# Kernel optimization log

Measured on AMD Instinct MI355X. Metric: run time of the kernel, lower is better.

## Reference

```python
import jax, jax.numpy as jnp
import numpy as np

EPS = 1e-12


def _pchip_slopes(y, x):
    """PCHIP (Fritsch-Carlson) slopes. y: (S, K), x: (K) -> (S, K)."""
    K = y.shape[-1]
    if K < 2:
        return jnp.zeros_like(y)
    h = x[1:] - x[:-1]                              # (K-1,)
    delta = (y[..., 1:] - y[..., :-1]) / (h + EPS)  # (S, K-1)
    if K == 2:
        return jnp.broadcast_to(delta[..., :1], y.shape).astype(y.dtype)
    # interior slopes: weighted harmonic mean where secants agree in sign
    delta_prev = delta[..., :-1]
    delta_next = delta[..., 1:]
    same_sign = delta_prev * delta_next > 0
    h_prev = h[:-1]
    h_next = h[1:]
    w1 = 2.0 * h_next + h_prev
    w2 = h_next + 2.0 * h_prev
    denom = w1 / (delta_prev + EPS) + w2 / (delta_next + EPS)
    d_int = (w1 + w2) / (denom + EPS)
    d_mid = jnp.where(same_sign, d_int, jnp.zeros_like(d_int))  # (S, K-2)
    # left endpoint (one-sided, shape-limited)
    h0, h1 = h[0], h[1]
    delta0 = delta[..., 0]
    delta1 = delta[..., 1]
    d0 = ((2.0 * h0 + h1) * delta0 - h0 * delta1) / (h0 + h1 + EPS)
    d0 = jnp.where(jnp.sign(d0) != jnp.sign(delta0), jnp.zeros_like(d0), d0)
    d0 = jnp.where((jnp.sign(delta0) != jnp.sign(delta1)) & (jnp.abs(d0) > 3.0 * jnp.abs(delta0)), 3.0 * delta0, d0)
    # right endpoint
    hn1, hn2 = h[-1], h[-2]
    deltan1 = delta[..., -1]
    deltan2 = delta[..., -2]
    dn = ((2.0 * hn1 + hn2) * deltan1 - hn1 * deltan2) / (hn1 + hn2 + EPS)
    dn = jnp.where(jnp.sign(dn) != jnp.sign(deltan1), jnp.zeros_like(dn), dn)
    dn = jnp.where((jnp.sign(deltan1) != jnp.sign(deltan2)) & (jnp.abs(dn) > 3.0 * jnp.abs(deltan1)), 3.0 * deltan1, dn)
    return jnp.concatenate([d0[..., None], d_mid, dn[..., None]], axis=-1)


def setup_inputs() -> dict:
    key = jax.random.key(0)
    k1, k2 = jax.random.split(key)
    B, S, K = 4096, 4096, 64
    x_min, x_max = -3.0, 3.0
    xq = jax.random.normal(k1, (B, S), dtype=jnp.float32) * 2.0  # some queries outside domain
    coeffs = jax.random.normal(k2, (S, K), dtype=jnp.float32)
    knots = jnp.linspace(x_min, x_max, K, dtype=jnp.float32)
    return {"xq": xq, "coeffs": coeffs, "knots": knots}


def reference(xq, coeffs, knots):
    y = coeffs                                   # (S, K)
    d = _pchip_slopes(y, knots)                  # (S, K)
    K = knots.shape[0]
    x0_dom = knots[0]
    x1_dom = knots[-1]
    below = xq < x0_dom
    above = xq > x1_dom
    xq_c = jnp.clip(xq, x0_dom, x1_dom)
    idx = jnp.searchsorted(knots, xq_c) - 1      # (B, S) interval index
    idx = jnp.clip(idx, 0, K - 2)
    x0 = knots[idx]
    x1 = knots[idx + 1]
    h = x1 - x0 + EPS
    t = (xq_c - x0) / h
    t2 = t * t
    t3 = t2 * t
    h00 = 2.0 * t3 - 3.0 * t2 + 1.0
    h10 = t3 - 2.0 * t2 + t
    h01 = -2.0 * t3 + 3.0 * t2
    h11 = t3 - t2
    s_idx = jnp.arange(y.shape[0])[None, :]      # (1, S) spline index
    y0 = y[s_idx, idx]
    y1 = y[s_idx, idx + 1]
    d0 = d[s_idx, idx]
    d1 = d[s_idx, idx + 1]
    interp = h00 * y0 + h10 * h * d0 + h01 * y1 + h11 * h * d1
    out = jnp.where(below, y[None, :, 0] + d[None, :, 0] * (xq - x0_dom), interp)
    out = jnp.where(above, y[None, :, -1] + d[None, :, -1] * (xq - x1_dom), out)
    return out
```

## Files before the change

### kernel.cpp

```cpp
#include <hip/hip_runtime.h>

#define EPSF 1e-12f
#define STILE 64
#define KK 64
#define RSTR 65
#define FSTR (4 * RSTR)
#define BLK 1024
#define NWAVE (BLK / 64)
#define PRELOOP ((STILE * KK) / BLK)

__device__ __forceinline__ float sgnf(float x) {
    return (x > 0.f) ? 1.f : ((x < 0.f) ? -1.f : 0.f);
}

__device__ __forceinline__ float4 eval4(float4 xv, const float4* __restrict__ qb,
                                        float af, float bf) {
    float xs[4] = {xv.x, xv.y, xv.z, xv.w};
    float t[4], ext[4];
    float4 c[4];
#pragma unroll
    for (int j = 0; j < 4; j++) {
        float tf = fmaf(xs[j], af, bf);
        float tc = fminf(fmaxf(tf, 0.f), (float)(KK - 1));
        int id = min((int)tc, KK - 2);
        t[j] = tc - (float)id;
        ext[j] = tf - tc;
        c[j] = qb[j * RSTR + id];
    }
    float r[4];
#pragma unroll
    for (int j = 0; j < 4; j++) {
        float P = fmaf(fmaf(fmaf(c[j].w, t[j], c[j].z), t[j], c[j].y), t[j], c[j].x);
        float w = fmaf(fmaf(t[j], 2.f, t[j]), c[j].w, c[j].z + c[j].z);
        float Pp = fmaf(t[j], w, c[j].y);
        r[j] = fmaf(Pp, ext[j], P);
    }
    return make_float4(r[0], r[1], r[2], r[3]);
}

__global__ __launch_bounds__(BLK, 8) void pchip_fused4(
    const float* __restrict__ xq,
    const float* __restrict__ coeffs,
    const float* __restrict__ knots,
    float* __restrict__ out,
    int S, int b_chunk)
{
    __shared__ float4 cf4[STILE * RSTR];
    __shared__ float skn[KK];
    float* cf = (float*)cf4;

    int tid = threadIdx.x;
    int s0 = blockIdx.x * STILE;
    int b0 = blockIdx.y * b_chunk;

    if (tid < KK) skn[tid] = knots[tid];
#pragma unroll
    for (int i = 0; i < PRELOOP; i++) {
        int p = tid + i * BLK;
        int sl = p >> 6, k = p & 63;
        cf[sl * FSTR + 4 * k] = coeffs[(size_t)(s0 + sl) * KK + k];
    }
    __syncthreads();
#pragma unroll
    for (int i = 0; i < PRELOOP; i++) {
        int p = tid + i * BLK;
        int sl = p >> 6, k = p & 63;
        if (k < KK - 1) {
            int ib = sl * FSTR + 4 * k;
            float hh = skn[k + 1] - skn[k];
            cf[ib + 3] = (cf[ib + 4] - cf[ib]) / (hh + EPSF);
        }
    }
    __syncthreads();
#pragma unroll
    for (int i = 0; i < PRELOOP; i++) {
        int p = tid + i * BLK;
        int sl = p >> 6, k = p & 63;
        int rb = sl * FSTR;
        float d;
        if (k == 0) {
            float h0 = skn[1] - skn[0], h1 = skn[2] - skn[1];
            float de0 = cf[rb + 3], de1 = cf[rb + 7];
            d = ((2.f * h0 + h1) * de0 - h0 * de1) / (h0 + h1 + EPSF);
            if (sgnf(d) != sgnf(de0)) d = 0.f;
            if ((sgnf(de0) != sgnf(de1)) && (fabsf(d) > 3.f * fabsf(de0))) d = 3.f * de0;
        } else if (k == KK - 1) {
            float hn1 = skn[KK - 1] - skn[KK - 2], hn2 = skn[KK - 2] - skn[KK - 3];
            float dn1 = cf[rb + 4 * (KK - 2) + 3], dn2 = cf[rb + 4 * (KK - 3) + 3];
            d = ((2.f * hn1 + hn2) * dn1 - hn1 * dn2) / (hn1 + hn2 + EPSF);
            if (sgnf(d) != sgnf(dn1)) d = 0.f;
            if ((sgnf(dn1) != sgnf(dn2)) && (fabsf(d) > 3.f * fabsf(dn1))) d = 3.f * dn1;
        } else {
            float dprev = cf[rb + 4 * (k - 1) + 3], dnext = cf[rb + 4 * k + 3];
            float hp = skn[k] - skn[k - 1], hn = skn[k + 1] - skn[k];
            bool same = dprev * dnext > 0.f;
            float w1 = 2.f * hn + hp;
            float w2 = hn + 2.f * hp;
            float denom = w1 / (dprev + EPSF) + w2 / (dnext + EPSF);
            float dint = (w1 + w2) / (denom + EPSF);
            d = same ? dint : 0.f;
        }
        cf[rb + 4 * k + 2] = d;
    }
    __syncthreads();
    float c1r[PRELOOP], c2r[PRELOOP], c3r[PRELOOP];
#pragma unroll
    for (int i = 0; i < PRELOOP; i++) {
        int p = tid + i * BLK;
        int sl = p >> 6, k = p & 63;
        int kc = min(k, KK - 2);
        int ib = sl * FSTR + 4 * kc;
        float y0 = cf[ib], y1 = cf[ib + 4];
        float d0 = cf[ib + 2], d1 = cf[ib + 6];
        float h = skn[kc + 1] - skn[kc] + EPSF;
        c1r[i] = h * d0;
        c2r[i] = 3.f * (y1 - y0) - h * (2.f * d0 + d1);
        c3r[i] = 2.f * (y0 - y1) + h * (d0 + d1);
    }
    __syncthreads();
#pragma unroll
    for (int i = 0; i < PRELOOP; i++) {
        int p = tid + i * BLK;
        int sl = p >> 6, k = p & 63;
        if (k < KK - 1) {
            int ib = sl * FSTR + 4 * k;
            cf[ib + 1] = c1r[i];
            cf[ib + 2] = c2r[i];
            cf[ib + 3] = c3r[i];
        }
    }
    __syncthreads();

    float x0d = skn[0], x1d = skn[KK - 1];
    float invh = (float)(KK - 1) / (x1d - x0d);
    float af = invh, bf = -x0d * invh;
    int wv = tid >> 6, lane = tid & 63;
    int cgrp = (lane & 15) << 2;
    int brw = lane >> 4;
    const float4* qb = cf4 + cgrp * RSTR;

    int rpw = b_chunk / NWAVE;
    int nb = rpw >> 2;
    size_t off = (size_t)(b0 + wv * rpw + brw) * S + s0 + cgrp;
    const size_t step = (size_t)4 * S;

    float4 xa = *(const float4*)(xq + off);
    float4 xb = *(const float4*)(xq + (nb > 1 ? off + step : off));
    for (int ii = 0; ii < nb; ii++) {
        float4 xn = *(const float4*)(xq + (ii + 2 < nb ? off + 2 * step : off));
        float4 r = eval4(xa, qb, af, bf);
        *(float4*)(out + off) = r;
        xa = xb; xb = xn;
        off += step;
    }
}

extern "C" void kernel_launch(void* const* d_in, const int* in_sizes, int n_in,
                              void* d_out, int out_size, void* d_ws, size_t ws_size,
                              hipStream_t stream) {
    const float* xq     = (const float*)d_in[0];
    const float* coeffs = (const float*)d_in[1];
    const float* knots  = (const float*)d_in[2];
    float* out = (float*)d_out;

    int K = in_sizes[2];
    int S = in_sizes[1] / K;
    int N = in_sizes[0];
    int B = N / S;

    int n_btiles = 8;
    int b_chunk = B / n_btiles;
    dim3 grid(S / STILE, n_btiles);
    pchip_fused4<<<grid, BLK, 0, stream>>>(xq, coeffs, knots, out, S, b_chunk);
}
```

Baseline: 126.9 us.

## Widen spline tile and software-pipeline LDS coefficient gathers with nontemporal stores

Doubles the spline tile to 128 columns so each wave covers 128 contiguous floats per row in two rows instead of four. The main loop is restructured so the interval index and LDS coefficient gather for the next row are issued before the Horner evaluation of the current one, with a scheduling barrier between them. Outputs are written with nontemporal stores. This is meant to hide LDS and global latency and reduce cache pollution, but it doubles LDS per block, so each CU holds fewer blocks, and it raises register pressure.

New measurement: 130.0 us. 2.4% more time.

```diff
diff --git a/kernel.cpp b/kernel.cpp
--- a/kernel.cpp
+++ b/kernel.cpp
@@ -1,7 +1,7 @@
 #include <hip/hip_runtime.h>
 
 #define EPSF 1e-12f
-#define STILE 64
+#define STILE 128
 #define KK 64
 #define RSTR 65
 #define FSTR (4 * RSTR)
@@ -9,25 +9,28 @@
 #define NWAVE (BLK / 64)
 #define PRELOOP ((STILE * KK) / BLK)
 
+typedef float f32x4 __attribute__((ext_vector_type(4)));
+
 __device__ __forceinline__ float sgnf(float x) {
     return (x > 0.f) ? 1.f : ((x < 0.f) ? -1.f : 0.f);
 }
 
-__device__ __forceinline__ float4 eval4(float4 xv, const float4* __restrict__ qb,
-                                        float af, float bf) {
+__device__ __forceinline__ void prep4(float4 xv, float af, float bf,
+                                      int* id, float* t, float* ext) {
     float xs[4] = {xv.x, xv.y, xv.z, xv.w};
-    float t[4], ext[4];
-    float4 c[4];
 #pragma unroll
     for (int j = 0; j < 4; j++) {
         float tf = fmaf(xs[j], af, bf);
         float tc = fminf(fmaxf(tf, 0.f), (float)(KK - 1));
-        int id = min((int)tc, KK - 2);
-        t[j] = tc - (float)id;
+        id[j] = min((int)tc, KK - 2);
+        t[j] = tc - (float)id[j];
         ext[j] = tf - tc;
-        c[j] = qb[j * RSTR + id];
     }
-    float r[4];
+}
+
+__device__ __forceinline__ f32x4 horner4(const float4* c, const float* t,
+                                         const float* ext) {
+    f32x4 r;
 #pragma unroll
     for (int j = 0; j < 4; j++) {
         float P = fmaf(fmaf(fmaf(c[j].w, t[j], c[j].z), t[j], c[j].y), t[j], c[j].x);
@@ -35,10 +38,10 @@
         float Pp = fmaf(t[j], w, c[j].y);
         r[j] = fmaf(Pp, ext[j], P);
     }
-    return make_float4(r[0], r[1], r[2], r[3]);
+    return r;
 }
 
-__global__ __launch_bounds__(BLK, 8) void pchip_fused4(
+__global__ __launch_bounds__(BLK, 4) void pchip_fused5(
     const float* __restrict__ xq,
     const float* __restrict__ coeffs,
     const float* __restrict__ knots,
@@ -135,22 +138,37 @@
     float invh = (float)(KK - 1) / (x1d - x0d);
     float af = invh, bf = -x0d * invh;
     int wv = tid >> 6, lane = tid & 63;
-    int cgrp = (lane & 15) << 2;
-    int brw = lane >> 4;
+    int cgrp = (lane & 31) << 2;
+    int brw = lane >> 5;
     const float4* qb = cf4 + cgrp * RSTR;
 
     int rpw = b_chunk / NWAVE;
-    int nb = rpw >> 2;
+    int nb = rpw >> 1;
     size_t off = (size_t)(b0 + wv * rpw + brw) * S + s0 + cgrp;
-    const size_t step = (size_t)4 * S;
+    const size_t step = (size_t)2 * S;
 
-    float4 xa = *(const float4*)(xq + off);
-    float4 xb = *(const float4*)(xq + (nb > 1 ? off + step : off));
+    float tc[4], ec[4], tn[4], en[4];
+    int idc[4], idn[4];
+    float4 cc[4], cn[4];
+    float4 xc = *(const float4*)(xq + off);
+    prep4(xc, af, bf, idc, tc, ec);
+#pragma unroll
+    for (int j = 0; j < 4; j++) cc[j] = qb[j * RSTR + idc[j]];
+    float4 xn = *(const float4*)(xq + (nb > 1 ? off + step : off));
+
     for (int ii = 0; ii < nb; ii++) {
-        float4 xn = *(const float4*)(xq + (ii + 2 < nb ? off + 2 * step : off));
-        float4 r = eval4(xa, qb, af, bf);
-        *(float4*)(out + off) = r;
-        xa = xb; xb = xn;
+        float4 xf = *(const float4*)(xq + (ii + 2 < nb ? off + 2 * step : off));
+        prep4(xn, af, bf, idn, tn, en);
+#pragma unroll
+        for (int j = 0; j < 4; j++) cn[j] = qb[j * RSTR + idn[j]];
+        __builtin_amdgcn_sched_barrier(0);
+        f32x4 r = horner4(cc, tc, ec);
+        __builtin_nontemporal_store(r, (f32x4*)(out + off));
+#pragma unroll
+        for (int j = 0; j < 4; j++) {
+            cc[j] = cn[j]; tc[j] = tn[j]; ec[j] = en[j];
+        }
+        xn = xf;
         off += step;
     }
 }
@@ -171,5 +189,5 @@
     int n_btiles = 8;
     int b_chunk = B / n_btiles;
     dim3 grid(S / STILE, n_btiles);
-    pchip_fused4<<<grid, BLK, 0, stream>>>(xq, coeffs, knots, out, S, b_chunk);
+    pchip_fused5<<<grid, BLK, 0, stream>>>(xq, coeffs, knots, out, S, b_chunk);
 }
```
